# Optimization experiments

Measured on AMD Instinct MI355X. Metric: run time of the kernel, lower is better.

The kernel has to match this reference:

```python
import jax, jax.numpy as jnp
import numpy as np

TEMP = 0.5
EPS = 1e-8  # matches torch F.cosine_similarity eps clamp


def setup_inputs() -> dict:
    key = jax.random.key(0)
    k1, k2 = jax.random.split(key)
    B, D = 8192, 512
    v = jax.random.normal(k1, (B, D), dtype=jnp.float32)
    u = jax.random.normal(k2, (B, D), dtype=jnp.float32)
    return {"v": v, "u": u}


def _normalize(x):
    n = jnp.sqrt(jnp.sum(x * x, axis=-1, keepdims=True))
    return x / jnp.maximum(n, EPS)


def reference(v, u):
    # Fused form of the original nested-loop NT-Xent-style loss.
    vn = _normalize(v)                      # [B, D]
    un = _normalize(u)                      # [B, D]
    sim = jnp.einsum('bd,cd->bc', vn, un)   # [B, B] pairwise cosine similarity
    diag = jnp.einsum('bd,bd->b', vn, un)   # cos(v_i, u_i)
    numerator = jnp.exp(diag / TEMP)        # [B]
    # original: denominator = numerator.detach().clone(); then += sum_j exp(sim[i,j]/T)
    denominator = jax.lax.stop_gradient(numerator) + jnp.sum(jnp.exp(sim / TEMP), axis=1)
    loss = -jnp.log(numerator / denominator)
    return loss
```

## Files before the change

### kernel.cpp

```cpp
#include <hip/hip_runtime.h>

typedef int   int4v  __attribute__((ext_vector_type(4)));
typedef char  char8v __attribute__((ext_vector_type(8)));

#define NROWS 8192
#define DIM 512
#define ROWB 512
#define NT 4
#define SWEEP 8

#define AS1(p) ((const __attribute__((address_space(1))) void*)(p))
#define AS3(p) ((__attribute__((address_space(3))) void*)(p))

#if __has_builtin(__builtin_amdgcn_exp2f)
#define EXP2(x) __builtin_amdgcn_exp2f(x)
#else
#define EXP2(x) exp2f(x)
#endif

__global__ __launch_bounds__(256) void prep_kernel(
    const float* __restrict__ v, const float* __restrict__ u,
    char* __restrict__ vq, char* __restrict__ uq,
    float* __restrict__ sa, float* __restrict__ sb,
    float* __restrict__ diag, float* __restrict__ rowsum)
{
    const int row  = blockIdx.x * 4 + (threadIdx.x >> 6);
    const int lane = threadIdx.x & 63;
    const float4* vr = reinterpret_cast<const float4*>(v + (size_t)row * DIM);
    const float4* ur = reinterpret_cast<const float4*>(u + (size_t)row * DIM);
    const float4 a0 = vr[lane * 2], a1 = vr[lane * 2 + 1];
    const float4 b0 = ur[lane * 2], b1 = ur[lane * 2 + 1];
    float av[8] = {a0.x, a0.y, a0.z, a0.w, a1.x, a1.y, a1.z, a1.w};
    float bv[8] = {b0.x, b0.y, b0.z, b0.w, b1.x, b1.y, b1.z, b1.w};
    float sv = 0.f, su = 0.f, sd = 0.f, mv = 0.f, mu = 0.f;
#pragma unroll
    for (int i = 0; i < 8; ++i) {
        sv += av[i] * av[i];
        su += bv[i] * bv[i];
        sd += av[i] * bv[i];
        mv = fmaxf(mv, fabsf(av[i]));
        mu = fmaxf(mu, fabsf(bv[i]));
    }
#pragma unroll
    for (int m = 32; m; m >>= 1) {
        sv += __shfl_xor(sv, m);
        su += __shfl_xor(su, m);
        sd += __shfl_xor(sd, m);
        mv = fmaxf(mv, __shfl_xor(mv, m));
        mu = fmaxf(mu, __shfl_xor(mu, m));
    }
    const float rv = 1.0f / fmaxf(sqrtf(sv), 1e-8f);
    const float ru = 1.0f / fmaxf(sqrtf(su), 1e-8f);
    const float qv = 127.0f / fmaxf(mv, 1e-20f);
    const float qu = 127.0f / fmaxf(mu, 1e-20f);
    char8v cv, cu;
#pragma unroll
    for (int i = 0; i < 8; ++i) {
        cv[i] = (char)__float2int_rn(av[i] * qv);
        cu[i] = (char)__float2int_rn(bv[i] * qu);
    }
    reinterpret_cast<char8v*>(vq + (size_t)row * DIM)[lane] = cv;
    reinterpret_cast<char8v*>(uq + (size_t)row * DIM)[lane] = cu;
    if (lane == 0) {
        sa[row] = mv * rv / 127.0f;
        sb[row] = mu * ru / 127.0f;
        diag[row] = sd * rv * ru;
        rowsum[row] = 0.0f;
    }
}

__global__ __launch_bounds__(256, 2) void simsum_kernel(
    const char* __restrict__ A, const char* __restrict__ Bq,
    const float* __restrict__ sa, const float* __restrict__ sb,
    float* __restrict__ rowsum)
{
    __shared__ __align__(16) char ldsB[4][16384];
    const int tid  = threadIdx.x;
    const int wave = tid >> 6;
    const int lane = tid & 63;
    const int ln15 = lane & 15;
    const int lhi  = lane >> 4;
    const int swz  = (ln15 & 7) << 4;

    const int brow = blockIdx.x;
    const int bgrp = blockIdx.y;
    const int growA = brow * 128 + wave * 32;
    const int gcol0 = bgrp * (SWEEP * 128);

    const char* gA = A;
    const char* gB = Bq;

    int4v Areg[NT][2][2];
#pragma unroll
    for (int t = 0; t < NT; ++t)
#pragma unroll
        for (int kk = 0; kk < 2; ++kk)
#pragma unroll
            for (int m = 0; m < 2; ++m) {
                const int r = growA + m * 16 + ln15;
                Areg[t][kk][m] = *reinterpret_cast<const int4v*>(
                    gA + (size_t)r * ROWB + t * 128 + kk * 64 + lhi * 16);
            }

    const float C2 = 2.885390081777927f;
    float ga[2][4];
#pragma unroll
    for (int m = 0; m < 2; ++m)
#pragma unroll
        for (int rr = 0; rr < 4; ++rr)
            ga[m][rr] = sa[growA + m * 16 + lhi * 4 + rr] * C2;

    float rs[2][4];
#pragma unroll
    for (int m = 0; m < 2; ++m)
#pragma unroll
        for (int rr = 0; rr < 4; ++rr)
            rs[m][rr] = 0.f;

    const int r0   = tid >> 3;
    const int sl16 = (((tid & 7) ^ ((tid >> 3) & 7)) << 4);

    auto stageB = [&](int bi, int gs) {
        const int ct = gs >> 2;
        const int kt = gs & 3;
#pragma unroll
        for (int q = 0; q < 4; ++q) {
            const int col = gcol0 + ct * 128 + q * 32 + r0;
            __builtin_amdgcn_global_load_lds(
                AS1(gB + (size_t)col * ROWB + kt * 128 + sl16),
                AS3(&ldsB[bi][q * 4096 + tid * 16]), 16, 0, 0);
        }
    };

    stageB(0, 0);
    stageB(1, 1);
    asm volatile("s_waitcnt vmcnt(4)" ::: "memory");
    asm volatile("s_barrier" ::: "memory");

    for (int s = 0; s < SWEEP; ++s) {
        int4v acc[2][8];
#pragma unroll
        for (int m = 0; m < 2; ++m)
#pragma unroll
            for (int n = 0; n < 8; ++n)
                acc[m][n] = (int4v){0, 0, 0, 0};

#pragma unroll
        for (int tt = 0; tt < NT; ++tt) {
            const int g = s * 4 + tt;
            if (g + 2 < 32) stageB((tt + 2) & 3, g + 2);
#pragma unroll
            for (int kk = 0; kk < 2; ++kk) {
                int4v Bf[8];
#pragma unroll
                for (int n = 0; n < 8; ++n) {
                    const int c = n * 16 + ln15;
                    Bf[n] = *reinterpret_cast<const int4v*>(
                        &ldsB[tt & 3][c * 128 + ((kk * 64 + lhi * 16) ^ swz)]);
                }
#pragma unroll
                for (int m = 0; m < 2; ++m)
#pragma unroll
                    for (int n = 0; n < 8; ++n)
                        acc[m][n] = __builtin_amdgcn_mfma_i32_16x16x64_i8(
                            Areg[tt][kk][m], Bf[n], acc[m][n], 0, 0, 0);
            }
            if (g < 30)       asm volatile("s_waitcnt vmcnt(4)" ::: "memory");
            else if (g == 30) asm volatile("s_waitcnt vmcnt(0)" ::: "memory");
            if (g < 31)       asm volatile("s_barrier" ::: "memory");
        }

        float sbv[8];
#pragma unroll
        for (int n = 0; n < 8; ++n)
            sbv[n] = sb[gcol0 + s * 128 + n * 16 + ln15];
#pragma unroll
        for (int m = 0; m < 2; ++m)
#pragma unroll
            for (int rr = 0; rr < 4; ++rr) {
                const float g2 = ga[m][rr];
#pragma unroll
                for (int n = 0; n < 8; ++n)
                    rs[m][rr] += EXP2((float)acc[m][n][rr] * g2 * sbv[n]);
            }
    }

#pragma unroll
    for (int m = 0; m < 2; ++m)
#pragma unroll
        for (int rr = 0; rr < 4; ++rr) {
            float s = rs[m][rr];
            s += __shfl_xor(s, 1);
            s += __shfl_xor(s, 2);
            s += __shfl_xor(s, 4);
            s += __shfl_xor(s, 8);
            if (ln15 == 0)
                atomicAdd(&rowsum[growA + m * 16 + lhi * 4 + rr], s);
        }
}

__global__ __launch_bounds__(256) void loss_kernel(
    const float* __restrict__ diag, const float* __restrict__ rowsum,
    float* __restrict__ out)
{
    const int i = blockIdx.x * 256 + threadIdx.x;
    const float d2 = diag[i] * 2.0f;
    out[i] = logf(expf(d2) + rowsum[i]) - d2;
}

extern "C" void kernel_launch(void* const* d_in, const int* in_sizes, int n_in,
                              void* d_out, int out_size, void* d_ws, size_t ws_size,
                              hipStream_t stream) {
    const float* v = (const float*)d_in[0];
    const float* u = (const float*)d_in[1];
    float* out = (float*)d_out;
    char* ws = (char*)d_ws;
    char*  vq     = ws;
    char*  uq     = ws + (size_t)4194304;
    float* sa     = (float*)(ws + (size_t)8388608);
    float* sb     = (float*)(ws + (size_t)8388608 + 32768);
    float* diag   = (float*)(ws + (size_t)8388608 + 65536);
    float* rowsum = (float*)(ws + (size_t)8388608 + 98304);

    prep_kernel<<<NROWS / 4, 256, 0, stream>>>(v, u, vq, uq, sa, sb, diag, rowsum);
    dim3 grid(64, 8);
    simsum_kernel<<<grid, 256, 0, stream>>>(vq, uq, sa, sb, rowsum);
    loss_kernel<<<NROWS / 256, 256, 0, stream>>>(diag, rowsum, out);
}
```

Baseline: 52.21 us.

## Halve B column tile per block, double grid, raise occupancy target

Shrinks the per-block B tile from 128 to 64 columns, which halves the LDS buffers and accumulator registers. It doubles the grid along the column dimension to 1024 blocks and raises launch bounds to 4 blocks per CU. The goal is more resident waves and better latency hiding on a grid that was small for the CU count. In exchange, each block reuses its A-register tile across fewer columns, total B traffic doubles, and rowsum atomics now happen per sweep instead of once per block, which adds atomic contention.

```diff
diff --git a/kernel.cpp b/kernel.cpp
--- a/kernel.cpp
+++ b/kernel.cpp
@@ -69,12 +69,12 @@
     }
 }
 
-__global__ __launch_bounds__(256, 2) void simsum_kernel(
+__global__ __launch_bounds__(256, 4) void simsum_kernel(
     const char* __restrict__ A, const char* __restrict__ Bq,
     const float* __restrict__ sa, const float* __restrict__ sb,
     float* __restrict__ rowsum)
 {
-    __shared__ __align__(16) char ldsB[4][16384];
+    __shared__ __align__(16) char ldsB[4][8192];
     const int tid  = threadIdx.x;
     const int wave = tid >> 6;
     const int lane = tid & 63;
@@ -85,10 +85,7 @@
     const int brow = blockIdx.x;
     const int bgrp = blockIdx.y;
     const int growA = brow * 128 + wave * 32;
-    const int gcol0 = bgrp * (SWEEP * 128);
-
-    const char* gA = A;
-    const char* gB = Bq;
+    const int gcol0 = bgrp * (SWEEP * 64);
 
     int4v Areg[NT][2][2];
 #pragma unroll
@@ -99,7 +96,7 @@
             for (int m = 0; m < 2; ++m) {
                 const int r = growA + m * 16 + ln15;
                 Areg[t][kk][m] = *reinterpret_cast<const int4v*>(
-                    gA + (size_t)r * ROWB + t * 128 + kk * 64 + lhi * 16);
+                    A + (size_t)r * ROWB + t * 128 + kk * 64 + lhi * 16);
             }
 
     const float C2 = 2.885390081777927f;
@@ -109,13 +106,6 @@
 #pragma unroll
         for (int rr = 0; rr < 4; ++rr)
             ga[m][rr] = sa[growA + m * 16 + lhi * 4 + rr] * C2;
-
-    float rs[2][4];
-#pragma unroll
-    for (int m = 0; m < 2; ++m)
-#pragma unroll
-        for (int rr = 0; rr < 4; ++rr)
-            rs[m][rr] = 0.f;
 
     const int r0   = tid >> 3;
     const int sl16 = (((tid & 7) ^ ((tid >> 3) & 7)) << 4);
@@ -124,25 +114,25 @@
         const int ct = gs >> 2;
         const int kt = gs & 3;
 #pragma unroll
-        for (int q = 0; q < 4; ++q) {
-            const int col = gcol0 + ct * 128 + q * 32 + r0;
+        for (int q = 0; q < 2; ++q) {
+            const int col = gcol0 + ct * 64 + q * 32 + r0;
             __builtin_amdgcn_global_load_lds(
-                AS1(gB + (size_t)col * ROWB + kt * 128 + sl16),
+                AS1(Bq + (size_t)col * ROWB + kt * 128 + sl16),
                 AS3(&ldsB[bi][q * 4096 + tid * 16]), 16, 0, 0);
         }
     };
 
     stageB(0, 0);
     stageB(1, 1);
-    asm volatile("s_waitcnt vmcnt(4)" ::: "memory");
+    asm volatile("s_waitcnt vmcnt(2)" ::: "memory");
     asm volatile("s_barrier" ::: "memory");
 
     for (int s = 0; s < SWEEP; ++s) {
-        int4v acc[2][8];
+        int4v acc[2][4];
 #pragma unroll
         for (int m = 0; m < 2; ++m)
 #pragma unroll
-            for (int n = 0; n < 8; ++n)
+            for (int n = 0; n < 4; ++n)
                 acc[m][n] = (int4v){0, 0, 0, 0};
 
 #pragma unroll
@@ -151,9 +141,9 @@
             if (g + 2 < 32) stageB((tt + 2) & 3, g + 2);
 #pragma unroll
             for (int kk = 0; kk < 2; ++kk) {
-                int4v Bf[8];
-#pragma unroll
-                for (int n = 0; n < 8; ++n) {
+                int4v Bf[4];
+#pragma unroll
+                for (int n = 0; n < 4; ++n) {
                     const int c = n * 16 + ln15;
                     Bf[n] = *reinterpret_cast<const int4v*>(
                         &ldsB[tt & 3][c * 128 + ((kk * 64 + lhi * 16) ^ swz)]);
@@ -161,42 +151,36 @@
 #pragma unroll
                 for (int m = 0; m < 2; ++m)
 #pragma unroll
-                    for (int n = 0; n < 8; ++n)
+                    for (int n = 0; n < 4; ++n)
                         acc[m][n] = __builtin_amdgcn_mfma_i32_16x16x64_i8(
                             Areg[tt][kk][m], Bf[n], acc[m][n], 0, 0, 0);
             }
-            if (g < 30)       asm volatile("s_waitcnt vmcnt(4)" ::: "memory");
+            if (g < 30)       asm volatile("s_waitcnt vmcnt(2)" ::: "memory");
             else if (g == 30) asm volatile("s_waitcnt vmcnt(0)" ::: "memory");
             if (g < 31)       asm volatile("s_barrier" ::: "memory");
         }
 
-        float sbv[8];
-#pragma unroll
-        for (int n = 0; n < 8; ++n)
-            sbv[n] = sb[gcol0 + s * 128 + n * 16 + ln15];
+        float sbv[4];
+#pragma unroll
+        for (int n = 0; n < 4; ++n)
+            sbv[n] = sb[gcol0 + s * 64 + n * 16 + ln15];
 #pragma unroll
         for (int m = 0; m < 2; ++m)
 #pragma unroll
             for (int rr = 0; rr < 4; ++rr) {
                 const float g2 = ga[m][rr];
-#pragma unroll
-                for (int n = 0; n < 8; ++n)
-                    rs[m][rr] += EXP2((float)acc[m][n][rr] * g2 * sbv[n]);
+                float sum = 0.f;
+#pragma unroll
+                for (int n = 0; n < 4; ++n)
+                    sum += EXP2((float)acc[m][n][rr] * g2 * sbv[n]);
+                sum += __shfl_xor(sum, 1);
+                sum += __shfl_xor(sum, 2);
+                sum += __shfl_xor(sum, 4);
+                sum += __shfl_xor(sum, 8);
+                if (ln15 == 0)
+                    atomicAdd(&rowsum[growA + m * 16 + lhi * 4 + rr], sum);
             }
     }
-
-#pragma unroll
-    for (int m = 0; m < 2; ++m)
-#pragma unroll
-        for (int rr = 0; rr < 4; ++rr) {
-            float s = rs[m][rr];
-            s += __shfl_xor(s, 1);
-            s += __shfl_xor(s, 2);
-            s += __shfl_xor(s, 4);
-            s += __shfl_xor(s, 8);
-            if (ln15 == 0)
-                atomicAdd(&rowsum[growA + m * 16 + lhi * 4 + rr], s);
-        }
 }
 
 __global__ __launch_bounds__(256) void loss_kernel(
@@ -223,7 +207,7 @@
     float* rowsum = (float*)(ws + (size_t)8388608 + 98304);
 
     prep_kernel<<<NROWS / 4, 256, 0, stream>>>(v, u, vq, uq, sa, sb, diag, rowsum);
-    dim3 grid(64, 8);
+    dim3 grid(64, 16);
     simsum_kernel<<<grid, 256, 0, stream>>>(vq, uq, sa, sb, rowsum);
     loss_kernel<<<NROWS / 256, 256, 0, stream>>>(diag, rowsum, out);
 }
```

Measured after the change: 67.96 us. +30.2%, slower.

## Halve sweep per block, triple-buffer LDS, raise occupancy to three blocks per CU

Applied to the files above, without the earlier changes.

Each block now sweeps 4 column tiles instead of 8, and the grid doubles to 64x16. The LDS staging ring drops from four buffers to three, and launch bounds ask for three blocks per CU. The per-row running sums are replaced by a reduction and atomicAdd after every sweep step, and the fully unrolled sweep loop lets the modulo-3 buffer indices resolve at compile time. The aim is more parallelism across the 256 CUs and higher occupancy, at the cost of more atomics, repeated A-register loads per block, and tighter register pressure.

```diff
diff --git a/kernel.cpp b/kernel.cpp
--- a/kernel.cpp
+++ b/kernel.cpp
@@ -7,7 +7,7 @@
 #define DIM 512
 #define ROWB 512
 #define NT 4
-#define SWEEP 8
+#define SWEEP 4
 
 #define AS1(p) ((const __attribute__((address_space(1))) void*)(p))
 #define AS3(p) ((__attribute__((address_space(3))) void*)(p))
@@ -69,12 +69,12 @@
     }
 }
 
-__global__ __launch_bounds__(256, 2) void simsum_kernel(
+__global__ __launch_bounds__(256, 3) void simsum_kernel(
     const char* __restrict__ A, const char* __restrict__ Bq,
     const float* __restrict__ sa, const float* __restrict__ sb,
     float* __restrict__ rowsum)
 {
-    __shared__ __align__(16) char ldsB[4][16384];
+    __shared__ __align__(16) char ldsB[3][16384];
     const int tid  = threadIdx.x;
     const int wave = tid >> 6;
     const int lane = tid & 63;
@@ -101,21 +101,6 @@
                 Areg[t][kk][m] = *reinterpret_cast<const int4v*>(
                     gA + (size_t)r * ROWB + t * 128 + kk * 64 + lhi * 16);
             }
-
-    const float C2 = 2.885390081777927f;
-    float ga[2][4];
-#pragma unroll
-    for (int m = 0; m < 2; ++m)
-#pragma unroll
-        for (int rr = 0; rr < 4; ++rr)
-            ga[m][rr] = sa[growA + m * 16 + lhi * 4 + rr] * C2;
-
-    float rs[2][4];
-#pragma unroll
-    for (int m = 0; m < 2; ++m)
-#pragma unroll
-        for (int rr = 0; rr < 4; ++rr)
-            rs[m][rr] = 0.f;
 
     const int r0   = tid >> 3;
     const int sl16 = (((tid & 7) ^ ((tid >> 3) & 7)) << 4);
@@ -137,6 +122,9 @@
     asm volatile("s_waitcnt vmcnt(4)" ::: "memory");
     asm volatile("s_barrier" ::: "memory");
 
+    const float C2 = 2.885390081777927f;
+
+#pragma unroll
     for (int s = 0; s < SWEEP; ++s) {
         int4v acc[2][8];
 #pragma unroll
@@ -148,7 +136,7 @@
 #pragma unroll
         for (int tt = 0; tt < NT; ++tt) {
             const int g = s * 4 + tt;
-            if (g + 2 < 32) stageB((tt + 2) & 3, g + 2);
+            if (g + 2 < 16) stageB((g + 2) % 3, g + 2);
 #pragma unroll
             for (int kk = 0; kk < 2; ++kk) {
                 int4v Bf[8];
@@ -156,7 +144,7 @@
                 for (int n = 0; n < 8; ++n) {
                     const int c = n * 16 + ln15;
                     Bf[n] = *reinterpret_cast<const int4v*>(
-                        &ldsB[tt & 3][c * 128 + ((kk * 64 + lhi * 16) ^ swz)]);
+                        &ldsB[g % 3][c * 128 + ((kk * 64 + lhi * 16) ^ swz)]);
                 }
 #pragma unroll
                 for (int m = 0; m < 2; ++m)
@@ -165,9 +153,9 @@
                         acc[m][n] = __builtin_amdgcn_mfma_i32_16x16x64_i8(
                             Areg[tt][kk][m], Bf[n], acc[m][n], 0, 0, 0);
             }
-            if (g < 30)       asm volatile("s_waitcnt vmcnt(4)" ::: "memory");
-            else if (g == 30) asm volatile("s_waitcnt vmcnt(0)" ::: "memory");
-            if (g < 31)       asm volatile("s_barrier" ::: "memory");
+            if (g < 14)       asm volatile("s_waitcnt vmcnt(4)" ::: "memory");
+            else if (g == 14) asm volatile("s_waitcnt vmcnt(0)" ::: "memory");
+            if (g < 15)       asm volatile("s_barrier" ::: "memory");
         }
 
         float sbv[8];
@@ -178,25 +166,20 @@
         for (int m = 0; m < 2; ++m)
 #pragma unroll
             for (int rr = 0; rr < 4; ++rr) {
-                const float g2 = ga[m][rr];
+                const int grow = growA + m * 16 + lhi * 4 + rr;
+                const float g2 = sa[grow] * C2;
+                float sum = 0.f;
 #pragma unroll
                 for (int n = 0; n < 8; ++n)
-                    rs[m][rr] += EXP2((float)acc[m][n][rr] * g2 * sbv[n]);
+                    sum += EXP2((float)acc[m][n][rr] * g2 * sbv[n]);
+                sum += __shfl_xor(sum, 1);
+                sum += __shfl_xor(sum, 2);
+                sum += __shfl_xor(sum, 4);
+                sum += __shfl_xor(sum, 8);
+                if (ln15 == 0)
+                    atomicAdd(&rowsum[grow], sum);
             }
     }
-
-#pragma unroll
-    for (int m = 0; m < 2; ++m)
-#pragma unroll
-        for (int rr = 0; rr < 4; ++rr) {
-            float s = rs[m][rr];
-            s += __shfl_xor(s, 1);
-            s += __shfl_xor(s, 2);
-            s += __shfl_xor(s, 4);
-            s += __shfl_xor(s, 8);
-            if (ln15 == 0)
-                atomicAdd(&rowsum[growA + m * 16 + lhi * 4 + rr], s);
-        }
 }
 
 __global__ __launch_bounds__(256) void loss_kernel(
@@ -223,7 +206,7 @@
     float* rowsum = (float*)(ws + (size_t)8388608 + 98304);
 
     prep_kernel<<<NROWS / 4, 256, 0, stream>>>(v, u, vq, uq, sa, sb, diag, rowsum);
-    dim3 grid(64, 8);
+    dim3 grid(64, 16);
     simsum_kernel<<<grid, 256, 0, stream>>>(vq, uq, sa, sb, rowsum);
     loss_kernel<<<NROWS / 256, 256, 0, stream>>>(diag, rowsum, out);
 }
```

Result: slower. 111.8 us (+114.2%).
